# Performance work log

Hardware: AMD Instinct MI355X
Metric: run time of the kernel (lower is better)

## Reference

```python
import jax, jax.numpy as jnp
import numpy as np

B, N, C, H = 4, 2048, 1024, 16
D = C // H

def setup_inputs() -> dict:
    key = jax.random.key(0)
    k1, k2, k3 = jax.random.split(key, 3)
    x = jax.random.normal(k1, (B, N, C), dtype=jnp.float32)
    w_qkv = jax.random.normal(k2, (C, 3 * C), dtype=jnp.float32) * (C ** -0.5)
    w_proj = jax.random.normal(k3, (C, C), dtype=jnp.float32) * (C ** -0.5)
    b_proj = jnp.zeros((C,), dtype=jnp.float32)
    return {"x": x, "w_qkv": w_qkv, "w_proj": w_proj, "b_proj": b_proj}

def reference(x, w_qkv, w_proj, b_proj):
    scale = D ** -0.5
    qkv = x @ w_qkv                                   # [B,N,3C]
    qkv = qkv.reshape(B, N, 3, H, D).transpose(2, 0, 3, 1, 4)  # [3,B,H,N,D]
    q, k, v = qkv[0], qkv[1], qkv[2]
    attn = jnp.einsum('bhnd,bhmd->bhnm', q, k) * scale  # [B,H,N,N]
    attn = jax.nn.softmax(attn, axis=-1)
    o = jnp.einsum('bhnm,bhmd->bhnd', attn, v)          # [B,H,N,D]
    o = o.transpose(0, 2, 1, 3).reshape(B, N, C)
    return o @ w_proj + b_proj
```

## Files before the change

kernel.cpp:

```cpp
#include <hip/hip_runtime.h>
#include <hip/hip_bf16.h>


#define B_ 4
#define N_ 2048
#define C_ 1024
#define H_ 16
#define D_ 64
#define MCONST 24.0f
#define QSCALE (0.125f * 1.44269504088896340736f)

typedef __attribute__((ext_vector_type(8))) __bf16 bf16x8;
typedef __attribute__((ext_vector_type(4))) float f32x4;
typedef __attribute__((ext_vector_type(16))) float f32x16;
typedef unsigned int u32;
typedef __attribute__((ext_vector_type(2))) u32 u32x2;
typedef __attribute__((ext_vector_type(4))) u32 u32x4;

__device__ inline unsigned short f2bf(float f) {
  __bf16 h = (__bf16)f;
  return __builtin_bit_cast(unsigned short, h);
}

__device__ __forceinline__ u32 pk2(float lo, float hi) {
  return (u32)f2bf(lo) | ((u32)f2bf(hi) << 16);
}

__device__ __forceinline__ void gld16(const void* g, void* l) {
  __builtin_amdgcn_global_load_lds(
      (const __attribute__((address_space(1))) u32*)g,
      (__attribute__((address_space(3))) u32*)l, 16, 0, 0);
}

__global__ __launch_bounds__(256) void cvt_bf16_kernel(
    const float* __restrict__ in, unsigned short* __restrict__ out) {
  int i = (blockIdx.x * 256 + threadIdx.x) * 8;
  float4 f0 = *(const float4*)&in[i];
  float4 f1 = *(const float4*)&in[i + 4];
  ushort4 h0, h1;
  h0.x = f2bf(f0.x); h0.y = f2bf(f0.y); h0.z = f2bf(f0.z); h0.w = f2bf(f0.w);
  h1.x = f2bf(f1.x); h1.y = f2bf(f1.y); h1.z = f2bf(f1.z); h1.w = f2bf(f1.w);
  *(ushort4*)&out[i] = h0;
  *(ushort4*)&out[i + 4] = h1;
}

__global__ __launch_bounds__(256) void transpose_cvt_kernel(
    const float* __restrict__ in, unsigned short* __restrict__ out,
    int K, int Nn) {
  __shared__ float tile[32][33];
  const int t = threadIdx.x;
  const int k0 = blockIdx.y * 32, n0 = blockIdx.x * 32;
  {
    int r = t >> 3, c = (t & 7) * 4;
    float4 f = *(const float4*)&in[(size_t)(k0 + r) * Nn + n0 + c];
    tile[r][c + 0] = f.x; tile[r][c + 1] = f.y;
    tile[r][c + 2] = f.z; tile[r][c + 3] = f.w;
  }
  __syncthreads();
  {
    int nr = t >> 3, kc = (t & 7) * 4;
    ushort4 h;
    h.x = f2bf(tile[kc + 0][nr]);
    h.y = f2bf(tile[kc + 1][nr]);
    h.z = f2bf(tile[kc + 2][nr]);
    h.w = f2bf(tile[kc + 3][nr]);
    *(ushort4*)&out[(size_t)(n0 + nr) * K + k0 + kc] = h;
  }
}

__global__ __launch_bounds__(512, 1) void gemm256_kernel(
    const unsigned short* __restrict__ A, const unsigned short* __restrict__ Bt,
    unsigned short* __restrict__ qb, unsigned short* __restrict__ kb,
    unsigned short* __restrict__ vtb, int M, int K, int Nout)
{
  __shared__ unsigned short LDS[3][2][256 * 32];
  const int tid = threadIdx.x;
  const int w = tid >> 6, lane = tid & 63;
  const int l15 = lane & 15, lk = lane >> 4;
  const int wm = w >> 2, wn = w & 3;
  const int n0 = blockIdx.x * 256, m0 = blockIdx.y * 256;

  const int s_row = tid >> 2;
  const int s_col = ((tid & 3) * 8) ^ (((s_row >> 3) & 1) * 16);
  const int s_dst = tid * 8;
  const int kcol = (lk * 8) ^ (((l15 >> 3) & 1) * 16);

  f32x4 acc[8][4];
#pragma unroll
  for (int m = 0; m < 8; m++)
#pragma unroll
    for (int n = 0; n < 4; n++) acc[m][n] = f32x4{0.f, 0.f, 0.f, 0.f};

#pragma unroll
  for (int i = 0; i < 2; i++)
    gld16(&A[(size_t)(m0 + i * 128 + s_row) * K + s_col],
          &LDS[0][0][i * 4096 + s_dst]);
#pragma unroll
  for (int i = 0; i < 2; i++)
    gld16(&Bt[(size_t)(n0 + i * 128 + s_row) * K + s_col],
          &LDS[0][1][i * 4096 + s_dst]);

  int cur = 0;
  for (int j = 0; j < 31; ++j) {
    const int nxt = (cur + 1 == 3) ? 0 : cur + 1;
    const int kt = (j + 1) * 32;
#pragma unroll
    for (int i = 0; i < 2; i++)
      gld16(&A[(size_t)(m0 + i * 128 + s_row) * K + kt + s_col],
            &LDS[nxt][0][i * 4096 + s_dst]);
    asm volatile("s_waitcnt vmcnt(2)" ::: "memory");
    __builtin_amdgcn_s_barrier();
    asm volatile("" ::: "memory");

    bf16x8 bf[4], af[4];
#pragma unroll
    for (int n = 0; n < 4; n++)
      bf[n] = *(const bf16x8*)&LDS[cur][1][(wn * 64 + n * 16 + l15) * 32 + kcol];
#pragma unroll
    for (int m = 0; m < 4; m++)
      af[m] = *(const bf16x8*)&LDS[cur][0][(wm * 128 + m * 16 + l15) * 32 + kcol];
    __builtin_amdgcn_s_setprio(1);
#pragma unroll
    for (int m = 0; m < 4; m++)
#pragma unroll
      for (int n = 0; n < 4; n++)
        acc[m][n] = __builtin_amdgcn_mfma_f32_16x16x32_bf16(af[m], bf[n], acc[m][n], 0, 0, 0);
    __builtin_amdgcn_s_setprio(0);

#pragma unroll
    for (int i = 0; i < 2; i++)
      gld16(&Bt[(size_t)(n0 + i * 128 + s_row) * K + kt + s_col],
            &LDS[nxt][1][i * 4096 + s_dst]);

#pragma unroll
    for (int m = 0; m < 4; m++)
      af[m] = *(const bf16x8*)&LDS[cur][0][(wm * 128 + (m + 4) * 16 + l15) * 32 + kcol];
    __builtin_amdgcn_s_setprio(1);
#pragma unroll
    for (int m = 0; m < 4; m++)
#pragma unroll
      for (int n = 0; n < 4; n++)
        acc[m + 4][n] = __builtin_amdgcn_mfma_f32_16x16x32_bf16(af[m], bf[n], acc[m + 4][n], 0, 0, 0);
    __builtin_amdgcn_s_setprio(0);
    cur = nxt;
  }

  asm volatile("s_waitcnt vmcnt(0)" ::: "memory");
  __builtin_amdgcn_s_barrier();
  asm volatile("" ::: "memory");
  {
    bf16x8 bf[4], af[4];
#pragma unroll
    for (int n = 0; n < 4; n++)
      bf[n] = *(const bf16x8*)&LDS[cur][1][(wn * 64 + n * 16 + l15) * 32 + kcol];
#pragma unroll
    for (int m = 0; m < 4; m++)
      af[m] = *(const bf16x8*)&LDS[cur][0][(wm * 128 + m * 16 + l15) * 32 + kcol];
#pragma unroll
    for (int m = 0; m < 4; m++)
#pragma unroll
      for (int n = 0; n < 4; n++)
        acc[m][n] = __builtin_amdgcn_mfma_f32_16x16x32_bf16(af[m], bf[n], acc[m][n], 0, 0, 0);
#pragma unroll
    for (int m = 0; m < 4; m++)
      af[m] = *(const bf16x8*)&LDS[cur][0][(wm * 128 + (m + 4) * 16 + l15) * 32 + kcol];
#pragma unroll
    for (int m = 0; m < 4; m++)
#pragma unroll
      for (int n = 0; n < 4; n++)
        acc[m + 4][n] = __builtin_amdgcn_mfma_f32_16x16x32_bf16(af[m], bf[n], acc[m + 4][n], 0, 0, 0);
  }

#pragma unroll
  for (int n = 0; n < 4; n++) {
    int c = n0 + wn * 64 + n * 16 + l15;
    int tsel = c >> 10, h = (c >> 6) & 15, d = c & 63;
    if (tsel < 2) {
      unsigned short* dst = (tsel == 0) ? qb : kb;
      float sc = (tsel == 0) ? QSCALE : 1.0f;
#pragma unroll
      for (int m = 0; m < 8; m++) {
#pragma unroll
        for (int r = 0; r < 4; r++) {
          int row = m0 + wm * 128 + m * 16 + lk * 4 + r;
          int b = row >> 11, nn = row & 2047;
          dst[(((size_t)(b * 16 + h)) * 2048 + nn) * 64 + d] = f2bf(acc[m][n][r] * sc);
        }
      }
    } else {
#pragma unroll
      for (int m = 0; m < 8; m++) {
        int row0 = m0 + wm * 128 + m * 16 + lk * 4;
        int b = row0 >> 11, nn = row0 & 2047;
        ushort4 pv;
        pv.x = f2bf(acc[m][n][0]); pv.y = f2bf(acc[m][n][1]);
        pv.z = f2bf(acc[m][n][2]); pv.w = f2bf(acc[m][n][3]);
        *(ushort4*)&vtb[(((size_t)(b * 16 + h)) * 64 + d) * 2048 + nn] = pv;
      }
    }
  }
}

__global__ __launch_bounds__(512, 1) void gemmproj_kernel(
    const unsigned short* __restrict__ A, const unsigned short* __restrict__ Bt,
    const float* __restrict__ bias, float* __restrict__ outp,
    int M, int K, int Nout)
{
  __shared__ unsigned short LDS[3][12288];
  const int tid = threadIdx.x;
  const int w = tid >> 6, lane = tid & 63;
  const int l15 = lane & 15, lk = lane >> 4;
  const int wm = w >> 1, wn = w & 1;
  const int n0 = blockIdx.x * 128, m0 = blockIdx.y * 256;

  const int s_row = tid >> 2;
  const int s_col = ((tid & 3) * 8) ^ (((s_row >> 3) & 1) * 16);
  const int s_dst = tid * 8;
  const int kcol = (lk * 8) ^ (((l15 >> 3) & 1) * 16);

  f32x4 acc[4][4];
#pragma unroll
  for (int m = 0; m < 4; m++)
#pragma unroll
    for (int n = 0; n < 4; n++) acc[m][n] = f32x4{0.f, 0.f, 0.f, 0.f};

#pragma unroll
  for (int i = 0; i < 2; i++)
    gld16(&A[(size_t)(m0 + i * 128 + s_row) * K + s_col],
          &LDS[0][i * 4096 + s_dst]);
  gld16(&Bt[(size_t)(n0 + s_row) * K + s_col], &LDS[0][8192 + s_dst]);

  int cur = 0;
  for (int j = 0; j < 31; ++j) {
    const int nxt = (cur + 1 == 3) ? 0 : cur + 1;
    const int kt = (j + 1) * 32;
#pragma unroll
    for (int i = 0; i < 2; i++)
      gld16(&A[(size_t)(m0 + i * 128 + s_row) * K + kt + s_col],
            &LDS[nxt][i * 4096 + s_dst]);
    asm volatile("s_waitcnt vmcnt(2)" ::: "memory");
    __builtin_amdgcn_s_barrier();
    asm volatile("" ::: "memory");

    bf16x8 bf[4], af[2];
#pragma unroll
    for (int n = 0; n < 4; n++)
      bf[n] = *(const bf16x8*)&LDS[cur][8192 + (wn * 64 + n * 16 + l15) * 32 + kcol];
#pragma unroll
    for (int m = 0; m < 2; m++)
      af[m] = *(const bf16x8*)&LDS[cur][(wm * 64 + m * 16 + l15) * 32 + kcol];
    __builtin_amdgcn_s_setprio(1);
#pragma unroll
    for (int m = 0; m < 2; m++)
#pragma unroll
      for (int n = 0; n < 4; n++)
        acc[m][n] = __builtin_amdgcn_mfma_f32_16x16x32_bf16(af[m], bf[n], acc[m][n], 0, 0, 0);
    __builtin_amdgcn_s_setprio(0);

    gld16(&Bt[(size_t)(n0 + s_row) * K + kt + s_col], &LDS[nxt][8192 + s_dst]);

#pragma unroll
    for (int m = 0; m < 2; m++)
      af[m] = *(const bf16x8*)&LDS[cur][(wm * 64 + (m + 2) * 16 + l15) * 32 + kcol];
    __builtin_amdgcn_s_setprio(1);
#pragma unroll
    for (int m = 0; m < 2; m++)
#pragma unroll
      for (int n = 0; n < 4; n++)
        acc[m + 2][n] = __builtin_amdgcn_mfma_f32_16x16x32_bf16(af[m], bf[n], acc[m + 2][n], 0, 0, 0);
    __builtin_amdgcn_s_setprio(0);
    cur = nxt;
  }

  asm volatile("s_waitcnt vmcnt(0)" ::: "memory");
  __builtin_amdgcn_s_barrier();
  asm volatile("" ::: "memory");
  {
    bf16x8 bf[4], af[2];
#pragma unroll
    for (int n = 0; n < 4; n++)
      bf[n] = *(const bf16x8*)&LDS[cur][8192 + (wn * 64 + n * 16 + l15) * 32 + kcol];
#pragma unroll
    for (int m = 0; m < 2; m++)
      af[m] = *(const bf16x8*)&LDS[cur][(wm * 64 + m * 16 + l15) * 32 + kcol];
#pragma unroll
    for (int m = 0; m < 2; m++)
#pragma unroll
      for (int n = 0; n < 4; n++)
        acc[m][n] = __builtin_amdgcn_mfma_f32_16x16x32_bf16(af[m], bf[n], acc[m][n], 0, 0, 0);
#pragma unroll
    for (int m = 0; m < 2; m++)
      af[m] = *(const bf16x8*)&LDS[cur][(wm * 64 + (m + 2) * 16 + l15) * 32 + kcol];
#pragma unroll
    for (int m = 0; m < 2; m++)
#pragma unroll
      for (int n = 0; n < 4; n++)
        acc[m + 2][n] = __builtin_amdgcn_mfma_f32_16x16x32_bf16(af[m], bf[n], acc[m + 2][n], 0, 0, 0);
  }

#pragma unroll
  for (int n = 0; n < 4; n++) {
    int c = n0 + wn * 64 + n * 16 + l15;
    float bv = bias[c];
#pragma unroll
    for (int m = 0; m < 4; m++) {
#pragma unroll
      for (int r = 0; r < 4; r++) {
        int row = m0 + wm * 64 + m * 16 + lk * 4 + r;
        outp[(size_t)row * Nout + c] = acc[m][n][r] + bv;
      }
    }
  }
}

__global__ __launch_bounds__(512) void flash_kernel(
    const unsigned short* __restrict__ qb, const unsigned short* __restrict__ kb,
    const unsigned short* __restrict__ vtb, unsigned short* __restrict__ ob)
{
  __shared__ unsigned short KVs[2][2][2][64 * 64];
  __shared__ float Lf[2][128];
  float* scratch = (float*)&KVs[0][0][0][0];

  const int tid = threadIdx.x;
  const int w = tid >> 6;
  const int lane = tid & 63;
  const int l31 = lane & 31;
  const int hi = lane >> 5;
  const int g = w >> 2;
  const int ws = w & 3;
  const int q0 = blockIdx.x * 128;
  const int bh = blockIdx.y;
  const size_t base = (size_t)bh * N_ * D_;
  const unsigned short* Qg = qb + base;
  const unsigned short* Kg = kb + base;
  const unsigned short* Vtg = vtb + base;

  const int t8 = tid & 255;
  const int s_r = t8 >> 3;
  const int s_sl = (t8 & 7) ^ (s_r & 7);
  const int swz = (lane & 7) << 3;

  const int qrow_g = q0 + ws * 32 + l31;
  bf16x8 qf[4];
#pragma unroll
  for (int ds = 0; ds < 4; ds++)
    qf[ds] = *(const bf16x8*)&Qg[(size_t)qrow_g * 64 + ds * 16 + hi * 8];

  f32x16 acc0, acc1, minit;
#pragma unroll
  for (int i = 0; i < 16; i++) { acc0[i] = 0.f; acc1[i] = 0.f; minit[i] = -MCONST; }
  float lrow = 0.f;

  const int kvbeg = g * (N_ / 2);

#pragma unroll
  for (int i = 0; i < 2; i++)
    gld16(&Kg[(size_t)(kvbeg + i * 32 + s_r) * 64 + s_sl * 8],
          &KVs[g][0][0][i * 2048 + ws * 512]);
#pragma unroll
  for (int i = 0; i < 2; i++)
    gld16(&Vtg[(size_t)(i * 32 + s_r) * N_ + kvbeg + s_sl * 8],
          &KVs[g][0][1][i * 2048 + ws * 512]);

  int cur = 0;
  for (int it = 0; it < 16; ++it) {
    __syncthreads();

    if (it + 1 < 16) {
      int kvn = kvbeg + (it + 1) * 64;
#pragma unroll
      for (int i = 0; i < 2; i++)
        gld16(&Kg[(size_t)(kvn + i * 32 + s_r) * 64 + s_sl * 8],
              &KVs[g][cur ^ 1][0][i * 2048 + ws * 512]);
#pragma unroll
      for (int i = 0; i < 2; i++)
        gld16(&Vtg[(size_t)(i * 32 + s_r) * N_ + kvn + s_sl * 8],
              &KVs[g][cur ^ 1][1][i * 2048 + ws * 512]);
    }

    const unsigned short* Kl = &KVs[g][cur][0][0];
    const unsigned short* Vl = &KVs[g][cur][1][0];

    u32 F[4][4];
#pragma unroll
    for (int t = 0; t < 2; t++) {
      f32x16 sa = minit;
      __builtin_amdgcn_s_setprio(1);
#pragma unroll
      for (int ds = 0; ds < 4; ds++) {
        bf16x8 a = *(const bf16x8*)&Kl[(t * 32 + l31) * 64 + ((ds * 16 + hi * 8) ^ swz)];
        sa = __builtin_amdgcn_mfma_f32_32x32x16_bf16(a, qf[ds], sa, 0, 0, 0);
      }
      __builtin_amdgcn_s_setprio(0);

      float p[16];
#pragma unroll
      for (int r = 0; r < 16; r++) p[r] = __builtin_amdgcn_exp2f(sa[r]);
      lrow += ((p[0] + p[1]) + (p[2] + p[3])) + ((p[4] + p[5]) + (p[6] + p[7]))
            + ((p[8] + p[9]) + (p[10] + p[11])) + ((p[12] + p[13]) + (p[14] + p[15]));

      u32 pk[8];
#pragma unroll
      for (int j = 0; j < 8; j++) pk[j] = pk2(p[2 * j], p[2 * j + 1]);
#if __has_builtin(__builtin_amdgcn_permlane32_swap)
      u32x2 r02 = __builtin_amdgcn_permlane32_swap(pk[0], pk[2], false, false);
      u32x2 r13 = __builtin_amdgcn_permlane32_swap(pk[1], pk[3], false, false);
      u32x2 r46 = __builtin_amdgcn_permlane32_swap(pk[4], pk[6], false, false);
      u32x2 r57 = __builtin_amdgcn_permlane32_swap(pk[5], pk[7], false, false);
      F[2 * t][0] = r02[0]; F[2 * t][2] = r02[1];
      F[2 * t][1] = r13[0]; F[2 * t][3] = r13[1];
      F[2 * t + 1][0] = r46[0]; F[2 * t + 1][2] = r46[1];
      F[2 * t + 1][1] = r57[0]; F[2 * t + 1][3] = r57[1];
#else
      u32 sw[8];
#pragma unroll
      for (int j = 0; j < 8; j++) sw[j] = (u32)__shfl_xor((int)pk[j], 32);
      F[2 * t][0] = hi ? sw[2] : pk[0];
      F[2 * t][1] = hi ? sw[3] : pk[1];
      F[2 * t][2] = hi ? pk[2] : sw[0];
      F[2 * t][3] = hi ? pk[3] : sw[1];
      F[2 * t + 1][0] = hi ? sw[6] : pk[4];
      F[2 * t + 1][1] = hi ? sw[7] : pk[5];
      F[2 * t + 1][2] = hi ? pk[6] : sw[4];
      F[2 * t + 1][3] = hi ? pk[7] : sw[5];
#endif
    }

    __builtin_amdgcn_s_setprio(1);
#pragma unroll
    for (int ks = 0; ks < 4; ks++) {
      u32x4 fv = {F[ks][0], F[ks][1], F[ks][2], F[ks][3]};
      bf16x8 a = __builtin_bit_cast(bf16x8, fv);
      bf16x8 b0 = *(const bf16x8*)&Vl[(0 * 32 + l31) * 64 + ((ks * 16 + hi * 8) ^ swz)];
      acc0 = __builtin_amdgcn_mfma_f32_32x32x16_bf16(a, b0, acc0, 0, 0, 0);
      bf16x8 b1 = *(const bf16x8*)&Vl[(1 * 32 + l31) * 64 + ((ks * 16 + hi * 8) ^ swz)];
      acc1 = __builtin_amdgcn_mfma_f32_32x32x16_bf16(a, b1, acc1, 0, 0, 0);
    }
    __builtin_amdgcn_s_setprio(0);
    cur ^= 1;
  }

  float rs = lrow + __shfl_xor(lrow, 32);
  if (lane < 32) Lf[g][ws * 32 + l31] = rs;
  __syncthreads();

  if (g == 0) {
#pragma unroll
    for (int r = 0; r < 16; r++) {
      int qr = (r & 3) + 8 * (r >> 2) + 4 * hi;
      scratch[(ws * 32 + qr) * 64 + l31]      = acc0[r];
      scratch[(ws * 32 + qr) * 64 + 32 + l31] = acc1[r];
    }
  }
  __syncthreads();
  if (g == 1) {
    const int b = bh >> 4, h = bh & 15;
#pragma unroll
    for (int r = 0; r < 16; r++) {
      int qr = (r & 3) + 8 * (r >> 2) + 4 * hi;
      float inv = 1.0f / (Lf[0][ws * 32 + qr] + Lf[1][ws * 32 + qr]);
      float o0 = scratch[(ws * 32 + qr) * 64 + l31]      + acc0[r];
      float o1 = scratch[(ws * 32 + qr) * 64 + 32 + l31] + acc1[r];
      int nq = q0 + ws * 32 + qr;
      size_t ob0 = (((size_t)b * N_ + nq) * H_ + h) * D_;
      ob[ob0 + l31]      = f2bf(o0 * inv);
      ob[ob0 + 32 + l31] = f2bf(o1 * inv);
    }
  }
}

extern "C" void kernel_launch(void* const* d_in, const int* in_sizes, int n_in,
                              void* d_out, int out_size, void* d_ws, size_t ws_size,
                              hipStream_t stream) {
  const float* x      = (const float*)d_in[0];
  const float* w_qkv  = (const float*)d_in[1];
  const float* w_proj = (const float*)d_in[2];
  const float* b_proj = (const float*)d_in[3];
  float* out = (float*)d_out;

  const size_t qsz = (size_t)B_ * H_ * N_ * D_;
  unsigned short* qb     = (unsigned short*)d_ws;
  unsigned short* kb     = qb + qsz;
  unsigned short* vtb    = kb + qsz;
  unsigned short* xbf    = vtb + qsz;
  unsigned short* ob     = xbf;
  unsigned short* wqkv_t = xbf + qsz;
  unsigned short* wproj_t= wqkv_t + (size_t)3072 * 1024;

  cvt_bf16_kernel<<<4096, 256, 0, stream>>>(x, xbf);
  transpose_cvt_kernel<<<dim3(3072 / 32, 1024 / 32), 256, 0, stream>>>(w_qkv, wqkv_t, 1024, 3072);
  transpose_cvt_kernel<<<dim3(1024 / 32, 1024 / 32), 256, 0, stream>>>(w_proj, wproj_t, 1024, 1024);

  gemm256_kernel<<<dim3(3072 / 256, 8192 / 256), 512, 0, stream>>>(
      xbf, wqkv_t, qb, kb, vtb, 8192, 1024, 3072);

  flash_kernel<<<dim3(N_ / 128, B_ * H_), 512, 0, stream>>>(qb, kb, vtb, ob);

  gemmproj_kernel<<<dim3(1024 / 128, 8192 / 256), 512, 0, stream>>>(
      ob, wproj_t, b_proj, out, 8192, 1024, 1024);
}
```

Baseline: 212.6 us.

## Load K/V fragments directly from global memory in flash kernel, drop LDS staging

Rewrites the attention kernel so each wave reads its K and transposed-V MFMA fragments straight from global memory into registers, instead of staging double-buffered tiles in shared memory. It also removes the two-group split of the KV range, which eliminates the cross-group reduction through shared memory, and halves the block size to 256 threads. The aim is to cut LDS traffic and block-wide barriers. The cost is that each wave now fetches whole K/V tiles redundantly through the caches with strided V accesses, there is no explicit prefetch to hide global latency, and per-block parallelism over the KV sequence is lost.

```diff
diff --git a/kernel.cpp b/kernel.cpp
--- a/kernel.cpp
+++ b/kernel.cpp
@@ -313,21 +313,16 @@
   }
 }
 
-__global__ __launch_bounds__(512) void flash_kernel(
+__global__ __launch_bounds__(256) void flash_kernel(
     const unsigned short* __restrict__ qb, const unsigned short* __restrict__ kb,
     const unsigned short* __restrict__ vtb, unsigned short* __restrict__ ob)
 {
-  __shared__ unsigned short KVs[2][2][2][64 * 64];
-  __shared__ float Lf[2][128];
-  float* scratch = (float*)&KVs[0][0][0][0];
-
+  __shared__ float Lw[4][32];
   const int tid = threadIdx.x;
   const int w = tid >> 6;
   const int lane = tid & 63;
   const int l31 = lane & 31;
   const int hi = lane >> 5;
-  const int g = w >> 2;
-  const int ws = w & 3;
   const int q0 = blockIdx.x * 128;
   const int bh = blockIdx.y;
   const size_t base = (size_t)bh * N_ * D_;
@@ -335,12 +330,7 @@
   const unsigned short* Kg = kb + base;
   const unsigned short* Vtg = vtb + base;
 
-  const int t8 = tid & 255;
-  const int s_r = t8 >> 3;
-  const int s_sl = (t8 & 7) ^ (s_r & 7);
-  const int swz = (lane & 7) << 3;
-
-  const int qrow_g = q0 + ws * 32 + l31;
+  const int qrow_g = q0 + w * 32 + l31;
   bf16x8 qf[4];
 #pragma unroll
   for (int ds = 0; ds < 4; ds++)
@@ -351,48 +341,35 @@
   for (int i = 0; i < 16; i++) { acc0[i] = 0.f; acc1[i] = 0.f; minit[i] = -MCONST; }
   float lrow = 0.f;
 
-  const int kvbeg = g * (N_ / 2);
-
-#pragma unroll
-  for (int i = 0; i < 2; i++)
-    gld16(&Kg[(size_t)(kvbeg + i * 32 + s_r) * 64 + s_sl * 8],
-          &KVs[g][0][0][i * 2048 + ws * 512]);
-#pragma unroll
-  for (int i = 0; i < 2; i++)
-    gld16(&Vtg[(size_t)(i * 32 + s_r) * N_ + kvbeg + s_sl * 8],
-          &KVs[g][0][1][i * 2048 + ws * 512]);
-
-  int cur = 0;
-  for (int it = 0; it < 16; ++it) {
-    __syncthreads();
-
-    if (it + 1 < 16) {
-      int kvn = kvbeg + (it + 1) * 64;
-#pragma unroll
-      for (int i = 0; i < 2; i++)
-        gld16(&Kg[(size_t)(kvn + i * 32 + s_r) * 64 + s_sl * 8],
-              &KVs[g][cur ^ 1][0][i * 2048 + ws * 512]);
-#pragma unroll
-      for (int i = 0; i < 2; i++)
-        gld16(&Vtg[(size_t)(i * 32 + s_r) * N_ + kvn + s_sl * 8],
-              &KVs[g][cur ^ 1][1][i * 2048 + ws * 512]);
-    }
-
-    const unsigned short* Kl = &KVs[g][cur][0][0];
-    const unsigned short* Vl = &KVs[g][cur][1][0];
+  for (int kv0 = 0; kv0 < N_; kv0 += 64) {
+    bf16x8 kf[2][4];
+#pragma unroll
+    for (int t = 0; t < 2; t++)
+#pragma unroll
+      for (int ds = 0; ds < 4; ds++)
+        kf[t][ds] = *(const bf16x8*)&Kg[(size_t)(kv0 + t * 32 + l31) * 64 + ds * 16 + hi * 8];
+
+    bf16x8 vf[2][4];
+#pragma unroll
+    for (int dt = 0; dt < 2; dt++)
+#pragma unroll
+      for (int ks = 0; ks < 4; ks++)
+        vf[dt][ks] = *(const bf16x8*)&Vtg[(size_t)(dt * 32 + l31) * N_ + kv0 + ks * 16 + hi * 8];
+
+    f32x16 sa0 = minit, sa1 = minit;
+    __builtin_amdgcn_s_setprio(1);
+#pragma unroll
+    for (int ds = 0; ds < 4; ds++)
+      sa0 = __builtin_amdgcn_mfma_f32_32x32x16_bf16(kf[0][ds], qf[ds], sa0, 0, 0, 0);
+#pragma unroll
+    for (int ds = 0; ds < 4; ds++)
+      sa1 = __builtin_amdgcn_mfma_f32_32x32x16_bf16(kf[1][ds], qf[ds], sa1, 0, 0, 0);
+    __builtin_amdgcn_s_setprio(0);
 
     u32 F[4][4];
 #pragma unroll
     for (int t = 0; t < 2; t++) {
-      f32x16 sa = minit;
-      __builtin_amdgcn_s_setprio(1);
-#pragma unroll
-      for (int ds = 0; ds < 4; ds++) {
-        bf16x8 a = *(const bf16x8*)&Kl[(t * 32 + l31) * 64 + ((ds * 16 + hi * 8) ^ swz)];
-        sa = __builtin_amdgcn_mfma_f32_32x32x16_bf16(a, qf[ds], sa, 0, 0, 0);
-      }
-      __builtin_amdgcn_s_setprio(0);
-
+      const f32x16& sa = t ? sa1 : sa0;
       float p[16];
 #pragma unroll
       for (int r = 0; r < 16; r++) p[r] = __builtin_amdgcn_exp2f(sa[r]);
@@ -431,41 +408,24 @@
     for (int ks = 0; ks < 4; ks++) {
       u32x4 fv = {F[ks][0], F[ks][1], F[ks][2], F[ks][3]};
       bf16x8 a = __builtin_bit_cast(bf16x8, fv);
-      bf16x8 b0 = *(const bf16x8*)&Vl[(0 * 32 + l31) * 64 + ((ks * 16 + hi * 8) ^ swz)];
-      acc0 = __builtin_amdgcn_mfma_f32_32x32x16_bf16(a, b0, acc0, 0, 0, 0);
-      bf16x8 b1 = *(const bf16x8*)&Vl[(1 * 32 + l31) * 64 + ((ks * 16 + hi * 8) ^ swz)];
-      acc1 = __builtin_amdgcn_mfma_f32_32x32x16_bf16(a, b1, acc1, 0, 0, 0);
+      acc0 = __builtin_amdgcn_mfma_f32_32x32x16_bf16(a, vf[0][ks], acc0, 0, 0, 0);
+      acc1 = __builtin_amdgcn_mfma_f32_32x32x16_bf16(a, vf[1][ks], acc1, 0, 0, 0);
     }
     __builtin_amdgcn_s_setprio(0);
-    cur ^= 1;
   }
 
   float rs = lrow + __shfl_xor(lrow, 32);
-  if (lane < 32) Lf[g][ws * 32 + l31] = rs;
-  __syncthreads();
-
-  if (g == 0) {
-#pragma unroll
-    for (int r = 0; r < 16; r++) {
-      int qr = (r & 3) + 8 * (r >> 2) + 4 * hi;
-      scratch[(ws * 32 + qr) * 64 + l31]      = acc0[r];
-      scratch[(ws * 32 + qr) * 64 + 32 + l31] = acc1[r];
-    }
-  }
-  __syncthreads();
-  if (g == 1) {
-    const int b = bh >> 4, h = bh & 15;
-#pragma unroll
-    for (int r = 0; r < 16; r++) {
-      int qr = (r & 3) + 8 * (r >> 2) + 4 * hi;
-      float inv = 1.0f / (Lf[0][ws * 32 + qr] + Lf[1][ws * 32 + qr]);
-      float o0 = scratch[(ws * 32 + qr) * 64 + l31]      + acc0[r];
-      float o1 = scratch[(ws * 32 + qr) * 64 + 32 + l31] + acc1[r];
-      int nq = q0 + ws * 32 + qr;
-      size_t ob0 = (((size_t)b * N_ + nq) * H_ + h) * D_;
-      ob[ob0 + l31]      = f2bf(o0 * inv);
-      ob[ob0 + 32 + l31] = f2bf(o1 * inv);
-    }
+  if (lane < 32) Lw[w][l31] = rs;
+
+  const int b = bh >> 4, h = bh & 15;
+#pragma unroll
+  for (int r = 0; r < 16; r++) {
+    int qr = (r & 3) + 8 * (r >> 2) + 4 * hi;
+    float inv = 1.0f / Lw[w][qr];
+    int nq = q0 + w * 32 + qr;
+    size_t ob0 = (((size_t)b * N_ + nq) * H_ + h) * D_;
+    ob[ob0 + l31]      = f2bf(acc0[r] * inv);
+    ob[ob0 + 32 + l31] = f2bf(acc1[r] * inv);
   }
 }
 
@@ -494,7 +454,7 @@
   gemm256_kernel<<<dim3(3072 / 256, 8192 / 256), 512, 0, stream>>>(
       xbf, wqkv_t, qb, kb, vtb, 8192, 1024, 3072);
 
-  flash_kernel<<<dim3(N_ / 128, B_ * H_), 512, 0, stream>>>(qb, kb, vtb, ob);
+  flash_kernel<<<dim3(N_ / 128, B_ * H_), 256, 0, stream>>>(qb, kb, vtb, ob);
 
   gemmproj_kernel<<<dim3(1024 / 128, 8192 / 256), 512, 0, stream>>>(
       ob, wproj_t, b_proj, out, 8192, 1024, 1024);
```

After: 348.5 us. 63.9% more time.
